# Performance work log

Hardware: AMD Instinct MI355X
Metric: run time of the kernel (lower is better)

Reference implementation:

```python
import jax, jax.numpy as jnp
import numpy as np

B, N, E, H = 2, 1000, 2000, 128


def setup_inputs() -> dict:
    key = jax.random.key(0)
    k1, k2, k3, k4, k5 = jax.random.split(key, 5)
    node_state = jax.random.normal(k1, (B, N, H), dtype=jnp.float32)
    edge_vec = jax.random.normal(k2, (B, E, H), dtype=jnp.float32)
    node2edge = jax.random.uniform(k3, (B, E, N), dtype=jnp.float32)
    edge2node = jax.random.uniform(k4, (B, N, E), dtype=jnp.float32)
    # xavier_uniform for a (H, H, H) tensor: fan_in = H*H, fan_out = H (torch views last 2 dims)
    bound = float(np.sqrt(6.0 / (H + H * H)))
    edge_network = jax.random.uniform(k5, (H, H, H), dtype=jnp.float32, minval=-bound, maxval=bound)
    return {
        "node_state": node_state,
        "edge_vec": edge_vec,
        "node2edge": node2edge,
        "edge2node": edge2node,
        "edge_network": edge_network,
    }


def reference(node_state, edge_vec, node2edge, edge2node, edge_network):
    # node2edge_emb[b,e,h] = sum_n node2edge[b,e,n] * node_state[b,n,h]
    n2e_emb = jnp.einsum("ben,bnh->beh", node2edge, node_state)
    # per-edge dynamic weight W[b,e,i,j] = sum_h edge_vec[b,e,h] * edge_network[h,i,j],
    # applied to n2e_emb; fused into one contraction (grouped edge-conditioned conv).
    new_n2e = jnp.einsum("beh,hij,bej->bei", edge_vec, edge_network, n2e_emb)
    norm = jnp.sum(edge2node, axis=2, keepdims=True) + 1.0  # [B,N,1]
    agg = (jnp.einsum("bne,bei->bni", edge2node, new_n2e) + node_state) / norm
    return agg
```

## Files before the change

### kernel.cpp

```cpp
#include <hip/hip_runtime.h>
#include <hip/hip_bf16.h>
#include <stdint.h>

#define Bv 2
#define Nv 1000
#define Ev 2000
#define Hv 128

typedef __attribute__((ext_vector_type(8))) short bf16x8;
typedef __attribute__((ext_vector_type(4))) float f32x4;
typedef unsigned short u16;
typedef unsigned int u32;

static __device__ __forceinline__ u32 pack2bf(float a, float b) {
  union { __hip_bfloat162 h; u32 u; } c;
  c.h = __float22bfloat162_rn(make_float2(a, b));
  return c.u;
}
static __device__ __forceinline__ u16 cvt1bf(float a) {
  return (u16)(pack2bf(a, 0.f) & 0xffffu);
}

static __device__ __forceinline__ void gload_lds16(const void* g, void* l) {
  __builtin_amdgcn_global_load_lds(
      (const __attribute__((address_space(1))) void*)g,
      (__attribute__((address_space(3))) void*)l, 16, 0, 0);
}

__global__ void k_prep(const float* __restrict__ en, u16* __restrict__ enbf,
                       const float* __restrict__ ns, u16* __restrict__ nsT) {
  const int bid = blockIdx.x;
  const int t = threadIdx.x;
  if (bid < 1024) {
    size_t idx = ((size_t)bid * 256u + t) * 8u;
    const f32x4* p = (const f32x4*)(en + idx);
    f32x4 a = p[0], b = p[1];
    uint4 o;
    o.x = pack2bf(a.x, a.y);
    o.y = pack2bf(a.z, a.w);
    o.z = pack2bf(b.x, b.y);
    o.w = pack2bf(b.z, b.w);
    *(uint4*)(enbf + idx) = o;
  } else {
    __shared__ float tile[32][33];
    const int zb = bid - 1024;
    const int x = zb & 31, y = (zb >> 5) & 3, z = zb >> 7;
    const float* src = ns + (size_t)z * Nv * Hv;
    u16* dst = nsT + (size_t)z * Hv * 1024;
    const int r0 = x * 32, c0 = y * 32;
    const int tx = t & 31, ty = t >> 5;
#pragma unroll
    for (int rr = 0; rr < 4; ++rr) {
      int r = r0 + ty + rr * 8;
      int c = c0 + tx;
      float v = (r < Nv) ? src[(size_t)r * Hv + c] : 0.f;
      tile[ty + rr * 8][tx] = v;
    }
    __syncthreads();
#pragma unroll
    for (int rr = 0; rr < 4; ++rr) {
      int oc = c0 + ty + rr * 8;
      int orr = r0 + tx;
      dst[(size_t)oc * 1024 + orr] = cvt1bf(tile[tx][ty + rr * 8]);
    }
  }
}

template <int M, int KREAL, int KPAD, int NKC, int NMT, bool ROWSUM>
__launch_bounds__(256, 4)
__global__ void k_gemm_flat(const float* __restrict__ A, const u16* __restrict__ BT,
                            float* __restrict__ Cpart, float* __restrict__ nrmpart) {
  __shared__ u16 AL[64 * 136];
  __shared__ float rowsum[64];
  const int id = blockIdx.x;
  const int kcid = id % NKC;
  const int mt = (id / NKC) % NMT;
  const int b = id / (NKC * NMT);
  A     += (size_t)b * M * KREAL;
  BT    += (size_t)b * 128 * KPAD;
  Cpart += (size_t)kcid * (2 * M * 128) + (size_t)b * M * 128;
  if (ROWSUM) nrmpart += (size_t)kcid * (2 * M) + (size_t)b * M;
  const int t = threadIdx.x;
  const int lane = t & 63;
  const int w = t >> 6;
  const int row16 = lane & 15;
  const int kg = lane >> 4;
  const int mrow0 = mt * 64;
  const int kc = kcid * 128;
  const int mtg = (w >> 1) * 2;
  const int itg = (w & 1) * 4;
  f32x4 acc[2][4];
#pragma unroll
  for (int i = 0; i < 2; ++i)
#pragma unroll
    for (int j = 0; j < 4; ++j) acc[i][j] = (f32x4){0.f, 0.f, 0.f, 0.f};
  if (ROWSUM && t < 64) rowsum[t] = 0.f;
  __syncthreads();
#pragma unroll
  for (int r = 0; r < 4; ++r) {
    const int chunk = t + r * 256;
    const int m = chunk >> 4;
    const int jc = (chunk & 15) * 8;
    const int gm = mrow0 + m;
    const int gk = kc + jc;
    f32x4 x0 = {0.f, 0.f, 0.f, 0.f}, x1 = {0.f, 0.f, 0.f, 0.f};
    if (gm < M && gk + 8 <= KREAL) {
      const f32x4* p = (const f32x4*)(A + (size_t)gm * KREAL + gk);
      x0 = p[0];
      x1 = p[1];
    }
    if (ROWSUM) {
      float s8 = x0.x + x0.y + x0.z + x0.w + x1.x + x1.y + x1.z + x1.w;
      s8 += __shfl_down(s8, 8, 16);
      s8 += __shfl_down(s8, 4, 16);
      s8 += __shfl_down(s8, 2, 16);
      s8 += __shfl_down(s8, 1, 16);
      if ((lane & 15) == 0) rowsum[m] += s8;
    }
    uint4 o;
    o.x = pack2bf(x0.x, x0.y);
    o.y = pack2bf(x0.z, x0.w);
    o.z = pack2bf(x1.x, x1.y);
    o.w = pack2bf(x1.z, x1.w);
    *(uint4*)&AL[m * 136 + jc] = o;
  }
  __syncthreads();
#pragma unroll
  for (int kk = 0; kk < 4; ++kk) {
    bf16x8 a[2], bfr[4];
#pragma unroll
    for (int q = 0; q < 2; ++q)
      a[q] = *(const bf16x8*)&AL[((mtg + q) * 16 + row16) * 136 + kk * 32 + kg * 8];
#pragma unroll
    for (int q = 0; q < 4; ++q)
      bfr[q] = *(const bf16x8*)(BT + (size_t)((itg + q) * 16 + row16) * KPAD + kc + kk * 32 + kg * 8);
#pragma unroll
    for (int mi = 0; mi < 2; ++mi)
#pragma unroll
      for (int ii = 0; ii < 4; ++ii)
        acc[mi][ii] = __builtin_amdgcn_mfma_f32_16x16x32_bf16(a[mi], bfr[ii], acc[mi][ii], 0, 0, 0);
  }
  if (ROWSUM && t < 64 && mrow0 + t < M) nrmpart[mrow0 + t] = rowsum[t];
#pragma unroll
  for (int mi = 0; mi < 2; ++mi) {
#pragma unroll
    for (int r = 0; r < 4; ++r) {
      const int lrow = (mtg + mi) * 16 + kg * 4 + r;
      const int gm = mrow0 + lrow;
      if (gm < M) {
#pragma unroll
        for (int ii = 0; ii < 4; ++ii)
          Cpart[(size_t)gm * 128 + (itg + ii) * 16 + row16] = acc[mi][ii][r];
      }
    }
  }
}

__global__ void k_reduce_emb(const float* __restrict__ part, u16* __restrict__ embbf) {
  const int tid = blockIdx.x * 256 + threadIdx.x;
  const size_t e = (size_t)tid * 8;
  const int b = (int)(e / 256000);
  const int rem = (int)(e % 256000);
  const int m = rem >> 7;
  const int j = rem & 127;
  const f32x4* p = (const f32x4*)part + tid * 2;
  f32x4 s0 = {0.f, 0.f, 0.f, 0.f}, s1 = {0.f, 0.f, 0.f, 0.f};
#pragma unroll
  for (int kc = 0; kc < 8; ++kc) {
    s0 += p[(size_t)kc * 128000];
    s1 += p[(size_t)kc * 128000 + 1];
  }
  uint4 o;
  o.x = pack2bf(s0.x, s0.y);
  o.y = pack2bf(s0.z, s0.w);
  o.z = pack2bf(s1.x, s1.y);
  o.w = pack2bf(s1.z, s1.w);
  *(uint4*)(embbf + ((size_t)b * 2048 + m) * 128 + j) = o;
}

__global__ void k_cvt_red(const float* __restrict__ part2, u16* __restrict__ neweT) {
  const int tid = blockIdx.x * 256 + threadIdx.x;
  const size_t f0 = (size_t)tid * 8;
  const int m0 = (int)(f0 & 2047);
  uint4 o;
  if (m0 >= Ev) {
    o = make_uint4(0, 0, 0, 0);
  } else {
    const f32x4* p = (const f32x4*)(part2 + f0);
    f32x4 s0 = {0.f, 0.f, 0.f, 0.f}, s1 = {0.f, 0.f, 0.f, 0.f};
#pragma unroll
    for (int hg = 0; hg < 8; ++hg) {
      s0 += p[(size_t)hg * 131072];
      s1 += p[(size_t)hg * 131072 + 1];
    }
    o.x = pack2bf(s0.x, s0.y);
    o.y = pack2bf(s0.z, s0.w);
    o.z = pack2bf(s1.x, s1.y);
    o.w = pack2bf(s1.z, s1.w);
  }
  *(uint4*)(neweT + f0) = o;
}

__global__ void k_epi_red(const float* __restrict__ part3, const float* __restrict__ nrmp,
                          const float* __restrict__ ns, float* __restrict__ out) {
  const int tid = blockIdx.x * 256 + threadIdx.x;
  const size_t f0 = (size_t)tid * 4;
  const int row = (int)(f0 >> 7);
  const f32x4* p = (const f32x4*)(part3 + f0);
  f32x4 s = {0.f, 0.f, 0.f, 0.f};
#pragma unroll
  for (int kc = 0; kc < 16; ++kc) s += p[(size_t)kc * 64000];
  float nm = 1.0f;
#pragma unroll
  for (int kc = 0; kc < 16; ++kc) nm += nrmp[(size_t)kc * 2000 + row];
  f32x4 nsv = *(const f32x4*)(ns + f0);
  *(f32x4*)(out + f0) = (s + nsv) * (1.0f / nm);
}

__launch_bounds__(256, 2)
__global__ void k_edge_mix(const float* __restrict__ ev, const u16* __restrict__ embbf,
                           const u16* __restrict__ enbf, float* __restrict__ part2) {
  __shared__ u16 APL[2][4][4096];
  __shared__ float EVL[64 * 20];
  const int id = blockIdx.x;
  const int hgrp = id & 7;
  const int rest = id >> 3;
  const int mt = rest & 31;
  const int b = rest >> 5;
  const int h0 = hgrp * 16;
  const int t = threadIdx.x;
  const int lane = t & 63;
  const int w = t >> 6;
  const int row16 = lane & 15;
  const int kg = lane >> 4;
  const int mbase = mt * 64;

  if (t < 64) {
    const int ml = mbase + t;
    const float* src = ev + ((size_t)b * Ev + ml) * Hv + h0;
    const f32x4 z = {0.f, 0.f, 0.f, 0.f};
#pragma unroll
    for (int q = 0; q < 4; ++q) {
      f32x4 v = (ml < Ev) ? *(const f32x4*)(src + q * 4) : z;
      *(f32x4*)&EVL[t * 20 + q * 4] = v;
    }
  }

  bf16x8 bfrag[4][4];
  {
    const u16* ebase = embbf + ((size_t)b * 2048 + mbase) * 128;
#pragma unroll
    for (int mf = 0; mf < 4; ++mf) {
      const u16* rp = ebase + (size_t)(mf * 16 + row16) * 128;
#pragma unroll
      for (int kk = 0; kk < 4; ++kk)
        bfrag[mf][kk] = *(const bf16x8*)(rp + kk * 32 + kg * 8);
    }
  }

  auto STAGE = [&](int p, int h) {
    const char* plane = (const char*)(enbf + (size_t)h * 16384) + (size_t)w * 8192;
    char* dst = (char*)&APL[p][w][0];
#pragma unroll
    for (int it = 0; it < 8; ++it) {
      const int r = it * 4 + (lane >> 4);
      const int inner = (lane & 15) << 4;
      const int srcb = r * 256 + (inner ^ ((r & 7) << 4));
      gload_lds16(plane + srcb, dst + it * 1024);
    }
  };

  const f32x4 zero4 = {0.f, 0.f, 0.f, 0.f};
  f32x4 pers[2][4];
#pragma unroll
  for (int fi = 0; fi < 2; ++fi)
#pragma unroll
    for (int mf = 0; mf < 4; ++mf) pers[fi][mf] = zero4;

  const int xorv = (row16 & 7) << 4;

  STAGE(0, h0);
  __syncthreads();

#pragma unroll 1
  for (int hh = 0; hh < 16; ++hh) {
    if (hh + 1 < 16) {
      STAGE((hh + 1) & 1, h0 + hh + 1);
      asm volatile("s_waitcnt vmcnt(8)" ::: "memory");
    } else {
      asm volatile("s_waitcnt vmcnt(0)" ::: "memory");
    }
    __builtin_amdgcn_sched_barrier(0);
    const char* sl = (const char*)&APL[hh & 1][w][0];
    bf16x8 a[2][4];
#pragma unroll
    for (int fi = 0; fi < 2; ++fi) {
      const int rs = fi * 16 + row16;
#pragma unroll
      for (int kk = 0; kk < 4; ++kk)
        a[fi][kk] = *(const bf16x8*)(sl + rs * 256 + ((kk * 64 + kg * 16) ^ xorv));
    }
    f32x4 q[2][4];
#pragma unroll
    for (int fi = 0; fi < 2; ++fi)
#pragma unroll
      for (int mf = 0; mf < 4; ++mf)
        q[fi][mf] = __builtin_amdgcn_mfma_f32_16x16x32_bf16(a[fi][0], bfrag[mf][0], zero4, 0, 0, 0);
#pragma unroll
    for (int kk = 1; kk < 4; ++kk)
#pragma unroll
      for (int fi = 0; fi < 2; ++fi)
#pragma unroll
        for (int mf = 0; mf < 4; ++mf)
          q[fi][mf] = __builtin_amdgcn_mfma_f32_16x16x32_bf16(a[fi][kk], bfrag[mf][kk], q[fi][mf], 0, 0, 0);
    float evv[4];
#pragma unroll
    for (int mf = 0; mf < 4; ++mf)
      evv[mf] = EVL[(mf * 16 + row16) * 20 + hh];
#pragma unroll
    for (int fi = 0; fi < 2; ++fi)
#pragma unroll
      for (int mf = 0; mf < 4; ++mf)
        pers[fi][mf] += evv[mf] * q[fi][mf];
  }

  float* slice = part2 + (size_t)hgrp * (2 * 128 * 2048);
#pragma unroll
  for (int fi = 0; fi < 2; ++fi) {
#pragma unroll
    for (int mf = 0; mf < 4; ++mf) {
      const int ml = mbase + mf * 16 + row16;
#pragma unroll
      for (int r = 0; r < 4; ++r) {
        const int irow = w * 32 + fi * 16 + kg * 4 + r;
        slice[((size_t)b * 128 + irow) * 2048 + ml] = pers[fi][mf][r];
      }
    }
  }
}

extern "C" void kernel_launch(void* const* d_in, const int* in_sizes, int n_in,
                              void* d_out, int out_size, void* d_ws, size_t ws_size,
                              hipStream_t stream) {
  const float* ns  = (const float*)d_in[0];
  const float* ev  = (const float*)d_in[1];
  const float* n2e = (const float*)d_in[2];
  const float* e2n = (const float*)d_in[3];
  const float* en  = (const float*)d_in[4];
  float* out = (float*)d_out;

  char* ws = (char*)d_ws;
  float* part1 = (float*)(ws);
  float* part2 = (float*)(ws + 16384000);
  float* part3 = (float*)(ws + 33161216);
  float* nrmp  = (float*)(ws + 49545216);
  u16*   embbf = (u16*)  (ws + 49673216);
  u16*   enbf  = (u16*)  (ws + 50721792);
  u16*   nsT   = (u16*)  (ws + 54916096);
  u16*   neweT = (u16*)  (ws + 55440384);

  k_prep<<<dim3(1280), dim3(256), 0, stream>>>(en, enbf, ns, nsT);
  k_gemm_flat<2000, 1000, 1024, 8, 32, false><<<dim3(512), dim3(256), 0, stream>>>(n2e, nsT, part1, nullptr);
  k_reduce_emb<<<dim3(250), dim3(256), 0, stream>>>(part1, embbf);
  k_edge_mix<<<dim3(512), dim3(256), 0, stream>>>(ev, embbf, enbf, part2);
  k_cvt_red<<<dim3(256), dim3(256), 0, stream>>>(part2, neweT);
  k_gemm_flat<1000, 2000, 2048, 16, 16, true><<<dim3(512), dim3(256), 0, stream>>>(e2n, neweT, part3, nrmp);
  k_epi_red<<<dim3(250), dim3(256), 0, stream>>>(part3, nrmp, ns, out);
}
```

Measured before the change: 67.20 us.

## Halve split-K partials via K-step loop and store edge-mix partials in bf16

The flat GEMM kernels now loop over two 128-wide K chunks per block, which halves the number of split-K partial buffers and the grid size (512 to 256 blocks). The reduce and epilogue kernels sum correspondingly fewer partials. Separately, the edge-mix partial outputs are written as bf16 instead of fp32, and k_cvt_red unpacks bf16 while summing. The goal is to cut the write and read traffic of the partial buffers. The trade-offs are less block-level parallelism, with 256 blocks for the GEMMs, and extra rounding of the per-group partials before they are summed.

Result: faster. 63.77 us (-5.1%).

```diff
diff --git a/kernel.cpp b/kernel.cpp
--- a/kernel.cpp
+++ b/kernel.cpp
@@ -66,7 +66,7 @@
   }
 }
 
-template <int M, int KREAL, int KPAD, int NKC, int NMT, bool ROWSUM>
+template <int M, int KREAL, int KPAD, int NKC, int KSTEPS, int NMT, bool ROWSUM>
 __launch_bounds__(256, 4)
 __global__ void k_gemm_flat(const float* __restrict__ A, const u16* __restrict__ BT,
                             float* __restrict__ Cpart, float* __restrict__ nrmpart) {
@@ -86,7 +86,6 @@
   const int row16 = lane & 15;
   const int kg = lane >> 4;
   const int mrow0 = mt * 64;
-  const int kc = kcid * 128;
   const int mtg = (w >> 1) * 2;
   const int itg = (w & 1) * 4;
   f32x4 acc[2][4];
@@ -95,50 +94,55 @@
 #pragma unroll
     for (int j = 0; j < 4; ++j) acc[i][j] = (f32x4){0.f, 0.f, 0.f, 0.f};
   if (ROWSUM && t < 64) rowsum[t] = 0.f;
-  __syncthreads();
-#pragma unroll
-  for (int r = 0; r < 4; ++r) {
-    const int chunk = t + r * 256;
-    const int m = chunk >> 4;
-    const int jc = (chunk & 15) * 8;
-    const int gm = mrow0 + m;
-    const int gk = kc + jc;
-    f32x4 x0 = {0.f, 0.f, 0.f, 0.f}, x1 = {0.f, 0.f, 0.f, 0.f};
-    if (gm < M && gk + 8 <= KREAL) {
-      const f32x4* p = (const f32x4*)(A + (size_t)gm * KREAL + gk);
-      x0 = p[0];
-      x1 = p[1];
-    }
-    if (ROWSUM) {
-      float s8 = x0.x + x0.y + x0.z + x0.w + x1.x + x1.y + x1.z + x1.w;
-      s8 += __shfl_down(s8, 8, 16);
-      s8 += __shfl_down(s8, 4, 16);
-      s8 += __shfl_down(s8, 2, 16);
-      s8 += __shfl_down(s8, 1, 16);
-      if ((lane & 15) == 0) rowsum[m] += s8;
-    }
-    uint4 o;
-    o.x = pack2bf(x0.x, x0.y);
-    o.y = pack2bf(x0.z, x0.w);
-    o.z = pack2bf(x1.x, x1.y);
-    o.w = pack2bf(x1.z, x1.w);
-    *(uint4*)&AL[m * 136 + jc] = o;
-  }
-  __syncthreads();
-#pragma unroll
-  for (int kk = 0; kk < 4; ++kk) {
-    bf16x8 a[2], bfr[4];
-#pragma unroll
-    for (int q = 0; q < 2; ++q)
-      a[q] = *(const bf16x8*)&AL[((mtg + q) * 16 + row16) * 136 + kk * 32 + kg * 8];
-#pragma unroll
-    for (int q = 0; q < 4; ++q)
-      bfr[q] = *(const bf16x8*)(BT + (size_t)((itg + q) * 16 + row16) * KPAD + kc + kk * 32 + kg * 8);
-#pragma unroll
-    for (int mi = 0; mi < 2; ++mi)
-#pragma unroll
-      for (int ii = 0; ii < 4; ++ii)
-        acc[mi][ii] = __builtin_amdgcn_mfma_f32_16x16x32_bf16(a[mi], bfr[ii], acc[mi][ii], 0, 0, 0);
+
+#pragma unroll 1
+  for (int s = 0; s < KSTEPS; ++s) {
+    const int kc = (kcid * KSTEPS + s) * 128;
+    __syncthreads();
+#pragma unroll
+    for (int r = 0; r < 4; ++r) {
+      const int chunk = t + r * 256;
+      const int m = chunk >> 4;
+      const int jc = (chunk & 15) * 8;
+      const int gm = mrow0 + m;
+      const int gk = kc + jc;
+      f32x4 x0 = {0.f, 0.f, 0.f, 0.f}, x1 = {0.f, 0.f, 0.f, 0.f};
+      if (gm < M && gk + 8 <= KREAL) {
+        const f32x4* p = (const f32x4*)(A + (size_t)gm * KREAL + gk);
+        x0 = p[0];
+        x1 = p[1];
+      }
+      if (ROWSUM) {
+        float s8 = x0.x + x0.y + x0.z + x0.w + x1.x + x1.y + x1.z + x1.w;
+        s8 += __shfl_down(s8, 8, 16);
+        s8 += __shfl_down(s8, 4, 16);
+        s8 += __shfl_down(s8, 2, 16);
+        s8 += __shfl_down(s8, 1, 16);
+        if ((lane & 15) == 0) rowsum[m] += s8;
+      }
+      uint4 o;
+      o.x = pack2bf(x0.x, x0.y);
+      o.y = pack2bf(x0.z, x0.w);
+      o.z = pack2bf(x1.x, x1.y);
+      o.w = pack2bf(x1.z, x1.w);
+      *(uint4*)&AL[m * 136 + jc] = o;
+    }
+    __syncthreads();
+#pragma unroll
+    for (int kk = 0; kk < 4; ++kk) {
+      bf16x8 a[2], bfr[4];
+#pragma unroll
+      for (int q = 0; q < 2; ++q)
+        a[q] = *(const bf16x8*)&AL[((mtg + q) * 16 + row16) * 136 + kk * 32 + kg * 8];
+#pragma unroll
+      for (int q = 0; q < 4; ++q)
+        bfr[q] = *(const bf16x8*)(BT + (size_t)((itg + q) * 16 + row16) * KPAD + kc + kk * 32 + kg * 8);
+#pragma unroll
+      for (int mi = 0; mi < 2; ++mi)
+#pragma unroll
+        for (int ii = 0; ii < 4; ++ii)
+          acc[mi][ii] = __builtin_amdgcn_mfma_f32_16x16x32_bf16(a[mi], bfr[ii], acc[mi][ii], 0, 0, 0);
+    }
   }
   if (ROWSUM && t < 64 && mrow0 + t < M) nrmpart[mrow0 + t] = rowsum[t];
 #pragma unroll
@@ -166,7 +170,7 @@
   const f32x4* p = (const f32x4*)part + tid * 2;
   f32x4 s0 = {0.f, 0.f, 0.f, 0.f}, s1 = {0.f, 0.f, 0.f, 0.f};
 #pragma unroll
-  for (int kc = 0; kc < 8; ++kc) {
+  for (int kc = 0; kc < 4; ++kc) {
     s0 += p[(size_t)kc * 128000];
     s1 += p[(size_t)kc * 128000 + 1];
   }
@@ -178,7 +182,7 @@
   *(uint4*)(embbf + ((size_t)b * 2048 + m) * 128 + j) = o;
 }
 
-__global__ void k_cvt_red(const float* __restrict__ part2, u16* __restrict__ neweT) {
+__global__ void k_cvt_red(const u16* __restrict__ part2, u16* __restrict__ neweT) {
   const int tid = blockIdx.x * 256 + threadIdx.x;
   const size_t f0 = (size_t)tid * 8;
   const int m0 = (int)(f0 & 2047);
@@ -186,17 +190,21 @@
   if (m0 >= Ev) {
     o = make_uint4(0, 0, 0, 0);
   } else {
-    const f32x4* p = (const f32x4*)(part2 + f0);
-    f32x4 s0 = {0.f, 0.f, 0.f, 0.f}, s1 = {0.f, 0.f, 0.f, 0.f};
+    float s[8] = {0.f, 0.f, 0.f, 0.f, 0.f, 0.f, 0.f, 0.f};
 #pragma unroll
     for (int hg = 0; hg < 8; ++hg) {
-      s0 += p[(size_t)hg * 131072];
-      s1 += p[(size_t)hg * 131072 + 1];
-    }
-    o.x = pack2bf(s0.x, s0.y);
-    o.y = pack2bf(s0.z, s0.w);
-    o.z = pack2bf(s1.x, s1.y);
-    o.w = pack2bf(s1.z, s1.w);
+      uint4 v = *(const uint4*)(part2 + (size_t)hg * 524288 + f0);
+      u32 wv[4] = {v.x, v.y, v.z, v.w};
+#pragma unroll
+      for (int q = 0; q < 4; ++q) {
+        s[2 * q]     += __uint_as_float(wv[q] << 16);
+        s[2 * q + 1] += __uint_as_float(wv[q] & 0xffff0000u);
+      }
+    }
+    o.x = pack2bf(s[0], s[1]);
+    o.y = pack2bf(s[2], s[3]);
+    o.z = pack2bf(s[4], s[5]);
+    o.w = pack2bf(s[6], s[7]);
   }
   *(uint4*)(neweT + f0) = o;
 }
@@ -209,17 +217,17 @@
   const f32x4* p = (const f32x4*)(part3 + f0);
   f32x4 s = {0.f, 0.f, 0.f, 0.f};
 #pragma unroll
-  for (int kc = 0; kc < 16; ++kc) s += p[(size_t)kc * 64000];
+  for (int kc = 0; kc < 8; ++kc) s += p[(size_t)kc * 64000];
   float nm = 1.0f;
 #pragma unroll
-  for (int kc = 0; kc < 16; ++kc) nm += nrmp[(size_t)kc * 2000 + row];
+  for (int kc = 0; kc < 8; ++kc) nm += nrmp[(size_t)kc * 2000 + row];
   f32x4 nsv = *(const f32x4*)(ns + f0);
   *(f32x4*)(out + f0) = (s + nsv) * (1.0f / nm);
 }
 
 __launch_bounds__(256, 2)
 __global__ void k_edge_mix(const float* __restrict__ ev, const u16* __restrict__ embbf,
-                           const u16* __restrict__ enbf, float* __restrict__ part2) {
+                           const u16* __restrict__ enbf, u16* __restrict__ part2) {
   __shared__ u16 APL[2][4][4096];
   __shared__ float EVL[64 * 20];
   const int id = blockIdx.x;
@@ -324,7 +332,7 @@
         pers[fi][mf] += evv[mf] * q[fi][mf];
   }
 
-  float* slice = part2 + (size_t)hgrp * (2 * 128 * 2048);
+  u16* slice = part2 + (size_t)hgrp * (2 * 128 * 2048);
 #pragma unroll
   for (int fi = 0; fi < 2; ++fi) {
 #pragma unroll
@@ -333,7 +341,7 @@
 #pragma unroll
       for (int r = 0; r < 4; ++r) {
         const int irow = w * 32 + fi * 16 + kg * 4 + r;
-        slice[((size_t)b * 128 + irow) * 2048 + ml] = pers[fi][mf][r];
+        slice[((size_t)b * 128 + irow) * 2048 + ml] = cvt1bf(pers[fi][mf][r]);
       }
     }
   }
@@ -351,19 +359,19 @@
 
   char* ws = (char*)d_ws;
   float* part1 = (float*)(ws);
-  float* part2 = (float*)(ws + 16384000);
-  float* part3 = (float*)(ws + 33161216);
-  float* nrmp  = (float*)(ws + 49545216);
-  u16*   embbf = (u16*)  (ws + 49673216);
-  u16*   enbf  = (u16*)  (ws + 50721792);
-  u16*   nsT   = (u16*)  (ws + 54916096);
-  u16*   neweT = (u16*)  (ws + 55440384);
+  u16*   part2 = (u16*)  (ws + 8192000);
+  float* part3 = (float*)(ws + 16580608);
+  float* nrmp  = (float*)(ws + 24772608);
+  u16*   embbf = (u16*)  (ws + 24838144);
+  u16*   enbf  = (u16*)  (ws + 25886720);
+  u16*   nsT   = (u16*)  (ws + 30081024);
+  u16*   neweT = (u16*)  (ws + 30605312);
 
   k_prep<<<dim3(1280), dim3(256), 0, stream>>>(en, enbf, ns, nsT);
-  k_gemm_flat<2000, 1000, 1024, 8, 32, false><<<dim3(512), dim3(256), 0, stream>>>(n2e, nsT, part1, nullptr);
+  k_gemm_flat<2000, 1000, 1024, 4, 2, 32, false><<<dim3(256), dim3(256), 0, stream>>>(n2e, nsT, part1, nullptr);
   k_reduce_emb<<<dim3(250), dim3(256), 0, stream>>>(part1, embbf);
   k_edge_mix<<<dim3(512), dim3(256), 0, stream>>>(ev, embbf, enbf, part2);
   k_cvt_red<<<dim3(256), dim3(256), 0, stream>>>(part2, neweT);
-  k_gemm_flat<1000, 2000, 2048, 16, 16, true><<<dim3(512), dim3(256), 0, stream>>>(e2n, neweT, part3, nrmp);
+  k_gemm_flat<1000, 2000, 2048, 8, 2, 16, true><<<dim3(256), dim3(256), 0, stream>>>(e2n, neweT, part3, nrmp);
   k_epi_red<<<dim3(250), dim3(256), 0, stream>>>(part3, nrmp, ns, out);
 }
```
